# Kernel optimization log

Measured on AMD Instinct MI355X. Metric: run time of the kernel, lower is better.

Reference implementation:

```python
import jax, jax.numpy as jnp
import numpy as np

B, N, PL = 8, 961, 50          # batch, sequence_len=(64-4)//2+1 squared, patch_len=3*4^2+2
HID = 200                       # int(4.0 * patch_len)
D, H, HD = 768, 12, 64          # embed_dim, num_heads, head_dim
MP = 1536                       # int(2.0 * embed_dim)


def setup_inputs() -> dict:
    key = jax.random.key(0)
    ks = jax.random.split(key, 16)
    w = lambda k, i, o: jax.random.normal(k, (i, o), jnp.float32) / np.float32(np.sqrt(i))
    b = lambda k, o: jax.random.normal(k, (o,), jnp.float32) * np.float32(0.01)
    return {
        "x": jax.random.normal(ks[0], (B, N, PL), jnp.float32),
        "W1": w(ks[1], PL, HID),   "b1": b(ks[2], HID),
        "W2": w(ks[3], HID, HID),  "b2": b(ks[4], HID),
        "W3": w(ks[5], HID, HID),  "b3": b(ks[6], HID),
        "W4": w(ks[7], HID, D),    "b4": b(ks[8], D),
        "Wruv": w(ks[9], D, 3 * D), "bruv": b(ks[10], 3 * D),
        "Wp1": w(ks[11], N * HD, MP), "bp1": b(ks[12], MP),
        "Wp2": w(ks[13], MP, 1),      "bp2": b(ks[14], 1),
    }


def reference(x, W1, b1, W2, b2, W3, b3, W4, b4, Wruv, bruv, Wp1, bp1, Wp2, bp2):
    Bs, Ns, _ = x.shape
    # pointwise MLP (note: original has NO activations, just stacked Linears)
    h = x.reshape(Bs * Ns, -1)
    h = (((h @ W1 + b1) @ W2 + b2) @ W3 + b3) @ W4 + b4           # (B*N, D)
    # fused r,u,v projection -> (3, H, B, N, HD)
    ruv = (h @ Wruv + bruv).reshape(Bs, Ns, 3, H, HD).transpose(2, 3, 0, 1, 4)
    r, u, v = ruv[0], ruv[1], ruv[2]                               # each (H, B, N, HD)
    attn = jax.nn.softmax(jnp.einsum('hbnd,hbmd->hbnm', r, u), axis=-1)
    o = jnp.einsum('hbnm,hbmd->hbnd', attn, v).reshape(H, Bs, Ns * HD)
    # per-head projection: weights are SHARED across heads (list built via [m]*H)
    q = (jnp.einsum('hbm,mp->hbp', o, Wp1) + bp1) @ Wp2 + bp2      # (H, B, 1)
    return q[..., 0].T                                             # (B, 12)
```

## Files before the change

### kernel.cpp

```cpp
#include <hip/hip_runtime.h>
#include <hip/hip_bf16.h>

#define TPB 256

typedef __attribute__((ext_vector_type(8))) short bf16x8;
typedef __attribute__((ext_vector_type(4))) float f32x4;

static __device__ __forceinline__ unsigned short f2bf(float f) {
  union { float f; unsigned int u; } x; x.f = f;
  unsigned int r = x.u + 0x7FFF + ((x.u >> 16) & 1);
  return (unsigned short)(r >> 16);
}
static __device__ __forceinline__ float bf2f(unsigned short h) {
  union { unsigned int u; float f; } x; x.u = ((unsigned int)h) << 16;
  return x.f;
}

#define MFMA16(a, b, c) __builtin_amdgcn_mfma_f32_16x16x32_bf16(a, b, c, 0, 0, 0)

__global__ __launch_bounds__(TPB) void gemm_fold_k(
    const float* __restrict__ A, const float* __restrict__ lastrow,
    const float* __restrict__ W, const float* __restrict__ bias,
    float* __restrict__ C, int K, int Nc)
{
  __shared__ float As[16][68];
  __shared__ float Ws[16][68];
  int tid = threadIdx.x;
  int col0 = blockIdx.x * 64;
  int ty = tid >> 4, tx = tid & 15;
  float acc[4][4] = {};
  for (int k0 = 0; k0 < K; k0 += 16) {
#pragma unroll
    for (int i = 0; i < 4; ++i) {
      int idx = tid + i * 256;
      int r = idx >> 4, kk = idx & 15;
      int gk = k0 + kk;
      float v = 0.f;
      if (gk < K) {
        if (r < 50) v = A[(size_t)r * K + gk];
        else if (r == 50) v = lastrow[gk];
      }
      As[kk][r] = v;
    }
#pragma unroll
    for (int i = 0; i < 4; ++i) {
      int idx = tid + i * 256;
      int c = idx & 63, kk = idx >> 6;
      int gc = col0 + c, gk = k0 + kk;
      float v = 0.f;
      if (gk < K && gc < Nc) v = W[(size_t)gk * Nc + gc];
      Ws[kk][c] = v;
    }
    __syncthreads();
#pragma unroll
    for (int kk = 0; kk < 16; ++kk) {
      float4 a4 = *(const float4*)&As[kk][ty * 4];
      float4 b4 = *(const float4*)&Ws[kk][tx * 4];
      float av[4] = {a4.x, a4.y, a4.z, a4.w};
      float bv[4] = {b4.x, b4.y, b4.z, b4.w};
#pragma unroll
      for (int i = 0; i < 4; ++i)
#pragma unroll
        for (int j = 0; j < 4; ++j)
          acc[i][j] = fmaf(av[i], bv[j], acc[i][j]);
    }
    __syncthreads();
  }
#pragma unroll
  for (int i = 0; i < 4; ++i) {
    int gr = ty * 4 + i;
    if (gr >= 51) continue;
#pragma unroll
    for (int j = 0; j < 4; ++j) {
      int gc = col0 + tx * 4 + j;
      if (gc >= Nc) continue;
      float v = acc[i][j];
      if (gr == 50) v += bias[gc];
      C[(size_t)gr * Nc + gc] = v;
    }
  }
}

__global__ __launch_bounds__(TPB) void fold4_xprep_k(
    const float* __restrict__ aug3,
    const float* __restrict__ Wruv,
    const float* __restrict__ bruv,
    unsigned short* __restrict__ WfTh, unsigned short* __restrict__ WfTl,
    float* __restrict__ bfv,
    const float* __restrict__ x,
    unsigned short* __restrict__ xh, unsigned short* __restrict__ xl)
{
  __shared__ float As[16][68];
  __shared__ float Ws[16][68];
  int bid = blockIdx.x;
  int tid = threadIdx.x;

  if (bid >= 36) {
    int row0 = (bid - 36) * 64;
#pragma unroll
    for (int i = 0; i < 16; ++i) {
      int idx = tid + i * 256;
      int row = row0 + (idx >> 6), cc = idx & 63;
      if (row >= 7688) continue;
      float v = (cc < 50) ? x[(size_t)row * 50 + cc] : 0.f;
      unsigned short hi = f2bf(v);
      xh[(size_t)row * 64 + cc] = hi;
      xl[(size_t)row * 64 + cc] = f2bf(v - bf2f(hi));
    }
    return;
  }

  const int K = 768, Nc = 2304;
  const float* lastrow = aug3 + (size_t)50 * 768;
  int col0 = bid * 64;
  int ty = tid >> 4, tx = tid & 15;
  float acc[4][4] = {};
  for (int k0 = 0; k0 < K; k0 += 16) {
#pragma unroll
    for (int i = 0; i < 4; ++i) {
      int idx = tid + i * 256;
      int r = idx >> 4, kk = idx & 15;
      int gk = k0 + kk;
      float v = 0.f;
      if (r < 50) v = aug3[(size_t)r * K + gk];
      else if (r == 50) v = lastrow[gk];
      As[kk][r] = v;
    }
#pragma unroll
    for (int i = 0; i < 4; ++i) {
      int idx = tid + i * 256;
      int c = idx & 63, kk = idx >> 6;
      Ws[kk][c] = Wruv[(size_t)(k0 + kk) * Nc + col0 + c];
    }
    __syncthreads();
#pragma unroll
    for (int kk = 0; kk < 16; ++kk) {
      float4 a4 = *(const float4*)&As[kk][ty * 4];
      float4 b4 = *(const float4*)&Ws[kk][tx * 4];
      float av[4] = {a4.x, a4.y, a4.z, a4.w};
      float bv[4] = {b4.x, b4.y, b4.z, b4.w};
#pragma unroll
      for (int i = 0; i < 4; ++i)
#pragma unroll
        for (int j = 0; j < 4; ++j)
          acc[i][j] = fmaf(av[i], bv[j], acc[i][j]);
    }
    __syncthreads();
  }
#pragma unroll
  for (int i = 0; i < 4; ++i) {
    int gr = ty * 4 + i;
    if (gr >= 51) continue;
#pragma unroll
    for (int j = 0; j < 4; ++j) {
      int gc = col0 + tx * 4 + j;
      float v = acc[i][j];
      if (gr == 50) {
        bfv[gc] = v + bruv[gc];
      } else {
        unsigned short hi = f2bf(v);
        size_t el = (size_t)gc * 64 + gr;
        WfTh[el] = hi;
        WfTl[el] = f2bf(v - bf2f(hi));
      }
    }
  }
}

__global__ __launch_bounds__(TPB) void gemm_ruv_mfma_k(
    const unsigned short* __restrict__ xh,
    const unsigned short* __restrict__ xl,
    const unsigned short* __restrict__ WfTh,
    const unsigned short* __restrict__ WfTl,
    const float* __restrict__ bias,
    unsigned short* __restrict__ RU,
    unsigned short* __restrict__ Vt)
{
  int tid = threadIdx.x, w = tid >> 6, lane = tid & 63;
  int g = lane >> 4, c = lane & 15;
  int by = blockIdx.y;
  int b = by >> 4, nb = by & 15;
  int m0 = b * 961 + nb * 64;
  int n0base = nb * 64;
  int col0 = blockIdx.x * 256;
  int wc0 = w * 64;

  bf16x8 afh[4][2], afl[4][2];
#pragma unroll
  for (int rt = 0; rt < 4; ++rt) {
    size_t rowb = (size_t)(m0 + rt * 16 + c) * 64;
#pragma unroll
    for (int kk = 0; kk < 2; ++kk) {
      afh[rt][kk] = *(const bf16x8*)&xh[rowb + kk * 32 + g * 8];
      afl[rt][kk] = *(const bf16x8*)&xl[rowb + kk * 32 + g * 8];
    }
  }

  f32x4 zero4 = {0.f, 0.f, 0.f, 0.f};
  f32x4 acc[4][4] = {{zero4, zero4, zero4, zero4}, {zero4, zero4, zero4, zero4},
                     {zero4, zero4, zero4, zero4}, {zero4, zero4, zero4, zero4}};

#pragma unroll
  for (int ct = 0; ct < 4; ++ct) {
    size_t bcolb = (size_t)(col0 + wc0 + ct * 16 + c) * 64;
    bf16x8 bh0 = *(const bf16x8*)&WfTh[bcolb + g * 8];
    bf16x8 bh1 = *(const bf16x8*)&WfTh[bcolb + 32 + g * 8];
    bf16x8 bl0 = *(const bf16x8*)&WfTl[bcolb + g * 8];
    bf16x8 bl1 = *(const bf16x8*)&WfTl[bcolb + 32 + g * 8];
#pragma unroll
    for (int rt = 0; rt < 4; ++rt) {
      acc[rt][ct] = MFMA16(afh[rt][0], bh0, acc[rt][ct]);
      acc[rt][ct] = MFMA16(afh[rt][1], bh1, acc[rt][ct]);
      acc[rt][ct] = MFMA16(afl[rt][0], bh0, acc[rt][ct]);
      acc[rt][ct] = MFMA16(afl[rt][1], bh1, acc[rt][ct]);
      acc[rt][ct] = MFMA16(afh[rt][0], bl0, acc[rt][ct]);
      acc[rt][ct] = MFMA16(afh[rt][1], bl1, acc[rt][ct]);
    }
  }

  bool isRU = (col0 < 1536);
#pragma unroll
  for (int ct = 0; ct < 4; ++ct) {
    int col = col0 + wc0 + ct * 16 + c;
    float bs = bias[col];
    if (isRU) {
#pragma unroll
      for (int rt = 0; rt < 4; ++rt) {
        int lr0 = rt * 16 + g * 4;
#pragma unroll
        for (int r = 0; r < 4; ++r) {
          int n = n0base + lr0 + r;
          if (n <= 960)
            RU[(size_t)(m0 + lr0 + r) * 1536 + col] = f2bf(acc[rt][ct][r] + bs);
        }
      }
    } else {
      int hd = col - 1536;
      int hh = hd >> 6, d = hd & 63;
      size_t vrow = ((size_t)(hh * 8 + b) * 64 + d) * 968;
#pragma unroll
      for (int rt = 0; rt < 4; ++rt) {
        int n0 = n0base + rt * 16 + g * 4;
        if (n0 + 3 <= 960) {
          ushort4 o;
          o.x = f2bf(acc[rt][ct][0] + bs);
          o.y = f2bf(acc[rt][ct][1] + bs);
          o.z = f2bf(acc[rt][ct][2] + bs);
          o.w = f2bf(acc[rt][ct][3] + bs);
          *(ushort4*)&Vt[vrow + n0] = o;
        } else {
#pragma unroll
          for (int r = 0; r < 4; ++r) {
            int n = n0 + r;
            if (n <= 960) Vt[vrow + n] = f2bf(acc[rt][ct][r] + bs);
          }
        }
      }
    }
  }
}

__global__ __launch_bounds__(512) void fold_wp_init_k(
    const float* __restrict__ Wp1, const float* __restrict__ Wp2,
    float* __restrict__ wfold,
    const float* __restrict__ bp1, const float* __restrict__ bp2,
    float* __restrict__ out)
{
  __shared__ float w2[1536];
  __shared__ float red[8];
  int bid = blockIdx.x;
  int tid = threadIdx.x;
  int wv = tid >> 6, lane = tid & 63;

  if (bid == 7688) {
    float s = 0.f;
    for (int i = tid; i < 1536; i += 512) s += bp1[i] * Wp2[i];
#pragma unroll
    for (int off = 32; off >= 1; off >>= 1) s += __shfl_xor(s, off, 64);
    if (lane == 0) red[wv] = s;
    __syncthreads();
    if (tid < 96) {
      float tot = red[0] + red[1] + red[2] + red[3] +
                  red[4] + red[5] + red[6] + red[7] + bp2[0];
      out[tid] = tot;
    }
    return;
  }

  for (int i = tid; i < 1536; i += 512) w2[i] = Wp2[i];
  __syncthreads();
  int m = bid * 8 + wv;
  const float* row = Wp1 + (size_t)m * 1536;
  float s = 0.f;
#pragma unroll
  for (int k = 0; k < 6; ++k) {
    float4 a  = *(const float4*)(row + k * 256 + lane * 4);
    float4 ww = *(const float4*)&w2[k * 256 + lane * 4];
    s += a.x * ww.x + a.y * ww.y + a.z * ww.z + a.w * ww.w;
  }
#pragma unroll
  for (int off = 32; off >= 1; off >>= 1) s += __shfl_xor(s, off, 64);
  if (lane == 0) wfold[m] = s;
}

__global__ __launch_bounds__(512) void attn_final_k(
    const unsigned short* __restrict__ RU,
    const unsigned short* __restrict__ Vt,
    const float* __restrict__ wfold,
    float* __restrict__ out)
{
  __shared__ unsigned short sh[24576];
  int bid = blockIdx.x;
  int tid = threadIdx.x;

  const int NS = 961, RS = 1536, VROW = 968;
  int qb = bid & 7, hb = bid >> 3;
  int h = hb >> 3, b = hb & 7;
  int n0 = qb * 128;
  int w = tid >> 6, lane = tid & 63;
  int g = lane >> 4, c = lane & 15;
  const unsigned short* rubase = RU + (size_t)b * NS * RS;
  int roff = h * 64, uoff = 768 + h * 64;
  const unsigned short* vtbase = Vt + (size_t)hb * 64 * VROW;
  unsigned short* Kbuf[2] = {sh, sh + 4096};
  unsigned short* Vbuf[2] = {sh + 8192, sh + 12288};
  unsigned short* pw = sh + 16384 + w * 1024;

  int qrow = n0 + w * 16 + c;
  if (qrow > 960) qrow = 960;
  bf16x8 qf0 = *(const bf16x8*)(rubase + (size_t)qrow * RS + roff + g * 8);
  bf16x8 qf1 = *(const bf16x8*)(rubase + (size_t)qrow * RS + roff + 32 + g * 8);

  bf16x8 ones;
#pragma unroll
  for (int i = 0; i < 8; ++i) ones[i] = (short)0x3F80;

  int srow = tid >> 3, ss = tid & 7;
  int sel = srow * 64 + 8 * (ss ^ (srow & 7));
  const unsigned short* ksrc = rubase + uoff + ss * 8;
  const unsigned short* vsrc = vtbase + (size_t)srow * VROW + ss * 8;

  {
    int4 kv = *(const int4*)(ksrc + (size_t)srow * RS);
    int4 vv = *(const int4*)(vsrc);
    *(int4*)&Kbuf[0][sel] = kv;
    *(int4*)&Vbuf[0][sel] = vv;
  }
  __syncthreads();

  f32x4 zero4 = {0.f, 0.f, 0.f, 0.f};
  f32x4 oacc[4] = {zero4, zero4, zero4, zero4};
  f32x4 rowacc = zero4;

  unsigned short* Kc = Kbuf[0];
  unsigned short* Vc = Vbuf[0];
  unsigned short* Kn = Kbuf[1];
  unsigned short* Vn = Vbuf[1];

  for (int kt = 0; kt < 16; ++kt) {
    int4 pk, pv;
    bool pre = (kt < 15);
    if (pre) {
      int keyg = (kt + 1) * 64 + srow;
      int kcl = keyg > 960 ? 960 : keyg;
      pk = *(const int4*)(ksrc + (size_t)kcl * RS);
      pv = *(const int4*)(vsrc + (kt + 1) * 64);
    }

    f32x4 sa[4] = {zero4, zero4, zero4, zero4};
    __builtin_amdgcn_s_setprio(1);
#pragma unroll
    for (int ct = 0; ct < 4; ++ct) {
      int key = c * 4 + ct;
      int sw = (key & 7) * 8;
      bf16x8 k0 = *(const bf16x8*)&Kc[key * 64 + ((g * 8) ^ sw)];
      bf16x8 k1 = *(const bf16x8*)&Kc[key * 64 + ((32 + g * 8) ^ sw)];
      sa[ct] = MFMA16(qf0, k0, sa[ct]);
      sa[ct] = MFMA16(qf1, k1, sa[ct]);
    }
    __builtin_amdgcn_s_setprio(0);

    if (kt < 15) {
#pragma unroll
      for (int r = 0; r < 4; ++r) {
        unsigned short pb[4];
#pragma unroll
        for (int ct = 0; ct < 4; ++ct)
          pb[ct] = f2bf(__expf(sa[ct][r]));
        int q = g * 4 + r;
        int e0 = (c * 4) ^ ((q & 7) * 8);
        *(unsigned int*)&pw[q * 64 + e0] =
            (unsigned int)pb[0] | ((unsigned int)pb[1] << 16);
        *(unsigned int*)&pw[q * 64 + e0 + 2] =
            (unsigned int)pb[2] | ((unsigned int)pb[3] << 16);
      }
    } else {
#pragma unroll
      for (int r = 0; r < 4; ++r) {
        unsigned short pb[4];
#pragma unroll
        for (int ct = 0; ct < 4; ++ct) {
          int keyg = kt * 64 + c * 4 + ct;
          pb[ct] = (keyg <= 960) ? f2bf(__expf(sa[ct][r])) : (unsigned short)0;
        }
        int q = g * 4 + r;
        int e0 = (c * 4) ^ ((q & 7) * 8);
        *(unsigned int*)&pw[q * 64 + e0] =
            (unsigned int)pb[0] | ((unsigned int)pb[1] << 16);
        *(unsigned int*)&pw[q * 64 + e0 + 2] =
            (unsigned int)pb[2] | ((unsigned int)pb[3] << 16);
      }
    }

    if (pre) {
      *(int4*)&Kn[sel] = pk;
      *(int4*)&Vn[sel] = pv;
    }

    __builtin_amdgcn_s_setprio(1);
#pragma unroll
    for (int kk = 0; kk < 2; ++kk) {
      bf16x8 pa = *(const bf16x8*)&pw[c * 64 + ((kk * 32 + g * 8) ^ ((c & 7) * 8))];
      rowacc = MFMA16(pa, ones, rowacc);
#pragma unroll
      for (int dt = 0; dt < 4; ++dt) {
        int d = dt * 16 + c;
        bf16x8 vf = *(const bf16x8*)&Vc[d * 64 + ((kk * 32 + g * 8) ^ ((d & 7) * 8))];
        oacc[dt] = MFMA16(pa, vf, oacc[dt]);
      }
    }
    __builtin_amdgcn_s_setprio(0);

    __syncthreads();
    unsigned short* t;
    t = Kc; Kc = Kn; Kn = t;
    t = Vc; Vc = Vn; Vn = t;
  }

  int nbase = n0 + w * 16 + g * 4;
  float part = 0.f;
#pragma unroll
  for (int r = 0; r < 4; ++r) {
    int n = nbase + r;
    if (n > 960) continue;
    float inv = 1.f / rowacc[r];
#pragma unroll
    for (int dt = 0; dt < 4; ++dt)
      part += oacc[dt][r] * inv * wfold[(size_t)n * 64 + dt * 16 + c];
  }
#pragma unroll
  for (int off = 32; off >= 1; off >>= 1) part += __shfl_xor(part, off, 64);
  float* red = (float*)sh;
  if (lane == 0) red[w] = part;
  __syncthreads();
  if (tid == 0) {
    float tot = red[0] + red[1] + red[2] + red[3] +
                red[4] + red[5] + red[6] + red[7];
    atomicAdd(&out[b * 12 + h], tot);
  }
}

extern "C" void kernel_launch(void* const* d_in, const int* in_sizes, int n_in,
                              void* d_out, int out_size, void* d_ws, size_t ws_size,
                              hipStream_t stream)
{
  const float* x    = (const float*)d_in[0];
  const float* W1   = (const float*)d_in[1];
  const float* b1   = (const float*)d_in[2];
  const float* W2   = (const float*)d_in[3];
  const float* b2   = (const float*)d_in[4];
  const float* W3   = (const float*)d_in[5];
  const float* b3   = (const float*)d_in[6];
  const float* W4   = (const float*)d_in[7];
  const float* b4   = (const float*)d_in[8];
  const float* Wruv = (const float*)d_in[9];
  const float* bruv = (const float*)d_in[10];
  const float* Wp1  = (const float*)d_in[11];
  const float* bp1  = (const float*)d_in[12];
  const float* Wp2  = (const float*)d_in[13];
  const float* bp2  = (const float*)d_in[14];
  float* out = (float*)d_out;

  char* base = (char*)d_ws;
  size_t off = 0;
  auto alloc = [&](size_t bytes) -> void* {
    void* p = base + off;
    off = (off + bytes + 255) & ~(size_t)255;
    return p;
  };
  unsigned short* RU  = (unsigned short*)alloc((size_t)7688 * 1536 * 2);
  unsigned short* Vt  = (unsigned short*)alloc((size_t)96 * 64 * 968 * 2 + 1024);
  float* aug1  = (float*)alloc(51 * 200 * 4);
  float* aug2  = (float*)alloc(51 * 200 * 4);
  float* aug3  = (float*)alloc(51 * 768 * 4);
  unsigned short* WfTh = (unsigned short*)alloc((size_t)2304 * 64 * 2);
  unsigned short* WfTl = (unsigned short*)alloc((size_t)2304 * 64 * 2);
  unsigned short* xh   = (unsigned short*)alloc((size_t)(7688 + 64) * 64 * 2);
  unsigned short* xl   = (unsigned short*)alloc((size_t)(7688 + 64) * 64 * 2);
  float* bfv   = (float*)alloc(2304 * 4);
  float* wfold = (float*)alloc(61504 * 4);
  if (off > ws_size) return;

  dim3 tb(TPB);

  gemm_fold_k<<<dim3(4),  tb, 0, stream>>>(W1,   b1,            W2, b2, aug1, 200, 200);
  gemm_fold_k<<<dim3(4),  tb, 0, stream>>>(aug1, aug1 + 50*200, W3, b3, aug2, 200, 200);
  gemm_fold_k<<<dim3(12), tb, 0, stream>>>(aug2, aug2 + 50*200, W4, b4, aug3, 200, 768);

  fold4_xprep_k<<<dim3(157), tb, 0, stream>>>(aug3, Wruv, bruv, WfTh, WfTl, bfv, x, xh, xl);

  gemm_ruv_mfma_k<<<dim3(9, 128), tb, 0, stream>>>(xh, xl, WfTh, WfTl, bfv, RU, Vt);

  fold_wp_init_k<<<dim3(7689), dim3(512), 0, stream>>>(Wp1, Wp2, wfold, bp1, bp2, out);

  attn_final_k<<<dim3(768), dim3(512), 0, stream>>>(RU, Vt, wfold, out);
}
```

Baseline: 383.4 us.

## Spread Wp1·Wp2 fold across the small fold GEMM launches and enlarge K tiles

The standalone Wp1×Wp2 folding kernel is removed. Its rows are split into chunks and handled by extra blocks appended to the three weight-fold GEMM launches and the fold4/xprep launch, so the bandwidth-bound Wp1 read runs alongside the tiny latency-bound GEMMs that previously left most CUs idle. The fold GEMMs also move from a K-tile of 16 to 64, which means fewer barriers but more shared memory per block (about 35 KB). The bias/out init moves into the first launch; 4-wave blocks now handle 4 rows each, so the fold work needs more blocks.

```diff
diff --git a/kernel.cpp b/kernel.cpp
--- a/kernel.cpp
+++ b/kernel.cpp
@@ -18,22 +18,59 @@
 
 #define MFMA16(a, b, c) __builtin_amdgcn_mfma_f32_16x16x32_bf16(a, b, c, 0, 0, 0)
 
-__global__ __launch_bounds__(TPB) void gemm_fold_k(
+__global__ __launch_bounds__(TPB) void fold_wp_fused_k(
     const float* __restrict__ A, const float* __restrict__ lastrow,
     const float* __restrict__ W, const float* __restrict__ bias,
-    float* __restrict__ C, int K, int Nc)
+    float* __restrict__ C, int K, int Nc, int gemmBlocks,
+    const float* __restrict__ Wp1, const float* __restrict__ Wp2,
+    float* __restrict__ wfold, int wpStart, int wpCount,
+    const float* __restrict__ bp1, const float* __restrict__ bp2,
+    float* __restrict__ out)
 {
-  __shared__ float As[16][68];
-  __shared__ float Ws[16][68];
-  int tid = threadIdx.x;
-  int col0 = blockIdx.x * 64;
+  __shared__ float As[64][68];
+  __shared__ float Ws[64][68];
+  __shared__ float red[4];
+  int bid = blockIdx.x, tid = threadIdx.x;
+
+  if (bid >= gemmBlocks) {
+    int u = bid - gemmBlocks;
+    int wv = tid >> 6, lane = tid & 63;
+    if (u >= wpCount) {
+      float s = 0.f;
+      for (int i = tid; i < 1536; i += TPB) s += bp1[i] * Wp2[i];
+#pragma unroll
+      for (int off = 32; off >= 1; off >>= 1) s += __shfl_xor(s, off, 64);
+      if (lane == 0) red[wv] = s;
+      __syncthreads();
+      if (tid < 96) out[tid] = red[0] + red[1] + red[2] + red[3] + bp2[0];
+      return;
+    }
+    float* w2 = &As[0][0];
+    for (int i = tid; i < 1536; i += TPB) w2[i] = Wp2[i];
+    __syncthreads();
+    int m = (wpStart + u) * 4 + wv;
+    const float* row = Wp1 + (size_t)m * 1536;
+    float s = 0.f;
+#pragma unroll
+    for (int k = 0; k < 6; ++k) {
+      float4 a  = *(const float4*)(row + k * 256 + lane * 4);
+      float4 ww = *(const float4*)&w2[k * 256 + lane * 4];
+      s += a.x * ww.x + a.y * ww.y + a.z * ww.z + a.w * ww.w;
+    }
+#pragma unroll
+    for (int off = 32; off >= 1; off >>= 1) s += __shfl_xor(s, off, 64);
+    if (lane == 0) wfold[m] = s;
+    return;
+  }
+
+  int col0 = bid * 64;
   int ty = tid >> 4, tx = tid & 15;
   float acc[4][4] = {};
-  for (int k0 = 0; k0 < K; k0 += 16) {
-#pragma unroll
-    for (int i = 0; i < 4; ++i) {
-      int idx = tid + i * 256;
-      int r = idx >> 4, kk = idx & 15;
+  for (int k0 = 0; k0 < K; k0 += 64) {
+#pragma unroll
+    for (int i = 0; i < 16; ++i) {
+      int idx = tid + i * TPB;
+      int r = idx >> 6, kk = idx & 63;
       int gk = k0 + kk;
       float v = 0.f;
       if (gk < K) {
@@ -43,17 +80,17 @@
       As[kk][r] = v;
     }
 #pragma unroll
-    for (int i = 0; i < 4; ++i) {
-      int idx = tid + i * 256;
-      int c = idx & 63, kk = idx >> 6;
-      int gc = col0 + c, gk = k0 + kk;
+    for (int i = 0; i < 16; ++i) {
+      int idx = tid + i * TPB;
+      int kk = idx >> 6, cc = idx & 63;
+      int gk = k0 + kk, gc = col0 + cc;
       float v = 0.f;
       if (gk < K && gc < Nc) v = W[(size_t)gk * Nc + gc];
-      Ws[kk][c] = v;
-    }
-    __syncthreads();
-#pragma unroll
-    for (int kk = 0; kk < 16; ++kk) {
+      Ws[kk][cc] = v;
+    }
+    __syncthreads();
+#pragma unroll 8
+    for (int kk = 0; kk < 64; ++kk) {
       float4 a4 = *(const float4*)&As[kk][ty * 4];
       float4 b4 = *(const float4*)&Ws[kk][tx * 4];
       float av[4] = {a4.x, a4.y, a4.z, a4.w};
@@ -81,25 +118,48 @@
   }
 }
 
-__global__ __launch_bounds__(TPB) void fold4_xprep_k(
+__global__ __launch_bounds__(TPB) void fold4_fused_k(
     const float* __restrict__ aug3,
     const float* __restrict__ Wruv,
     const float* __restrict__ bruv,
     unsigned short* __restrict__ WfTh, unsigned short* __restrict__ WfTl,
     float* __restrict__ bfv,
     const float* __restrict__ x,
-    unsigned short* __restrict__ xh, unsigned short* __restrict__ xl)
+    unsigned short* __restrict__ xh, unsigned short* __restrict__ xl,
+    const float* __restrict__ Wp1, const float* __restrict__ Wp2,
+    float* __restrict__ wfold, int wpStart, int wpCount)
 {
-  __shared__ float As[16][68];
-  __shared__ float Ws[16][68];
-  int bid = blockIdx.x;
-  int tid = threadIdx.x;
+  __shared__ float As[64][68];
+  __shared__ float Ws[64][68];
+  int bid = blockIdx.x, tid = threadIdx.x;
+
+  if (bid >= 157) {
+    int u = bid - 157;
+    if (u >= wpCount) return;
+    int wv = tid >> 6, lane = tid & 63;
+    float* w2 = &As[0][0];
+    for (int i = tid; i < 1536; i += TPB) w2[i] = Wp2[i];
+    __syncthreads();
+    int m = (wpStart + u) * 4 + wv;
+    const float* row = Wp1 + (size_t)m * 1536;
+    float s = 0.f;
+#pragma unroll
+    for (int k = 0; k < 6; ++k) {
+      float4 a  = *(const float4*)(row + k * 256 + lane * 4);
+      float4 ww = *(const float4*)&w2[k * 256 + lane * 4];
+      s += a.x * ww.x + a.y * ww.y + a.z * ww.z + a.w * ww.w;
+    }
+#pragma unroll
+    for (int off = 32; off >= 1; off >>= 1) s += __shfl_xor(s, off, 64);
+    if (lane == 0) wfold[m] = s;
+    return;
+  }
 
   if (bid >= 36) {
     int row0 = (bid - 36) * 64;
 #pragma unroll
     for (int i = 0; i < 16; ++i) {
-      int idx = tid + i * 256;
+      int idx = tid + i * TPB;
       int row = row0 + (idx >> 6), cc = idx & 63;
       if (row >= 7688) continue;
       float v = (cc < 50) ? x[(size_t)row * 50 + cc] : 0.f;
@@ -115,11 +175,11 @@
   int col0 = bid * 64;
   int ty = tid >> 4, tx = tid & 15;
   float acc[4][4] = {};
-  for (int k0 = 0; k0 < K; k0 += 16) {
-#pragma unroll
-    for (int i = 0; i < 4; ++i) {
-      int idx = tid + i * 256;
-      int r = idx >> 4, kk = idx & 15;
+  for (int k0 = 0; k0 < K; k0 += 64) {
+#pragma unroll
+    for (int i = 0; i < 16; ++i) {
+      int idx = tid + i * TPB;
+      int r = idx >> 6, kk = idx & 63;
       int gk = k0 + kk;
       float v = 0.f;
       if (r < 50) v = aug3[(size_t)r * K + gk];
@@ -127,14 +187,14 @@
       As[kk][r] = v;
     }
 #pragma unroll
-    for (int i = 0; i < 4; ++i) {
-      int idx = tid + i * 256;
-      int c = idx & 63, kk = idx >> 6;
-      Ws[kk][c] = Wruv[(size_t)(k0 + kk) * Nc + col0 + c];
-    }
-    __syncthreads();
-#pragma unroll
-    for (int kk = 0; kk < 16; ++kk) {
+    for (int i = 0; i < 16; ++i) {
+      int idx = tid + i * TPB;
+      int kk = idx >> 6, cc = idx & 63;
+      Ws[kk][cc] = Wruv[(size_t)(k0 + kk) * Nc + col0 + cc];
+    }
+    __syncthreads();
+#pragma unroll 8
+    for (int kk = 0; kk < 64; ++kk) {
       float4 a4 = *(const float4*)&As[kk][ty * 4];
       float4 b4 = *(const float4*)&Ws[kk][tx * 4];
       float av[4] = {a4.x, a4.y, a4.z, a4.w};
@@ -258,49 +318,6 @@
       }
     }
   }
-}
-
-__global__ __launch_bounds__(512) void fold_wp_init_k(
-    const float* __restrict__ Wp1, const float* __restrict__ Wp2,
-    float* __restrict__ wfold,
-    const float* __restrict__ bp1, const float* __restrict__ bp2,
-    float* __restrict__ out)
-{
-  __shared__ float w2[1536];
-  __shared__ float red[8];
-  int bid = blockIdx.x;
-  int tid = threadIdx.x;
-  int wv = tid >> 6, lane = tid & 63;
-
-  if (bid == 7688) {
-    float s = 0.f;
-    for (int i = tid; i < 1536; i += 512) s += bp1[i] * Wp2[i];
-#pragma unroll
-    for (int off = 32; off >= 1; off >>= 1) s += __shfl_xor(s, off, 64);
-    if (lane == 0) red[wv] = s;
-    __syncthreads();
-    if (tid < 96) {
-      float tot = red[0] + red[1] + red[2] + red[3] +
-                  red[4] + red[5] + red[6] + red[7] + bp2[0];
-      out[tid] = tot;
-    }
-    return;
-  }
-
-  for (int i = tid; i < 1536; i += 512) w2[i] = Wp2[i];
-  __syncthreads();
-  int m = bid * 8 + wv;
-  const float* row = Wp1 + (size_t)m * 1536;
-  float s = 0.f;
-#pragma unroll
-  for (int k = 0; k < 6; ++k) {
-    float4 a  = *(const float4*)(row + k * 256 + lane * 4);
-    float4 ww = *(const float4*)&w2[k * 256 + lane * 4];
-    s += a.x * ww.x + a.y * ww.y + a.z * ww.z + a.w * ww.w;
-  }
-#pragma unroll
-  for (int off = 32; off >= 1; off >>= 1) s += __shfl_xor(s, off, 64);
-  if (lane == 0) wfold[m] = s;
 }
 
 __global__ __launch_bounds__(512) void attn_final_k(
@@ -503,15 +520,21 @@
 
   dim3 tb(TPB);
 
-  gemm_fold_k<<<dim3(4),  tb, 0, stream>>>(W1,   b1,            W2, b2, aug1, 200, 200);
-  gemm_fold_k<<<dim3(4),  tb, 0, stream>>>(aug1, aug1 + 50*200, W3, b3, aug2, 200, 200);
-  gemm_fold_k<<<dim3(12), tb, 0, stream>>>(aug2, aug2 + 50*200, W4, b4, aug3, 200, 768);
-
-  fold4_xprep_k<<<dim3(157), tb, 0, stream>>>(aug3, Wruv, bruv, WfTh, WfTl, bfv, x, xh, xl);
+  fold_wp_fused_k<<<dim3(4 + 3000 + 1), tb, 0, stream>>>(
+      W1, b1, W2, b2, aug1, 200, 200, 4,
+      Wp1, Wp2, wfold, 0, 3000, bp1, bp2, out);
+  fold_wp_fused_k<<<dim3(4 + 3000), tb, 0, stream>>>(
+      aug1, aug1 + 50 * 200, W3, b3, aug2, 200, 200, 4,
+      Wp1, Wp2, wfold, 3000, 3000, bp1, bp2, out);
+  fold_wp_fused_k<<<dim3(12 + 3000), tb, 0, stream>>>(
+      aug2, aug2 + 50 * 200, W4, b4, aug3, 200, 768, 12,
+      Wp1, Wp2, wfold, 6000, 3000, bp1, bp2, out);
+
+  fold4_fused_k<<<dim3(157 + 6376), tb, 0, stream>>>(
+      aug3, Wruv, bruv, WfTh, WfTl, bfv, x, xh, xl,
+      Wp1, Wp2, wfold, 9000, 6376);
 
   gemm_ruv_mfma_k<<<dim3(9, 128), tb, 0, stream>>>(xh, xl, WfTh, WfTl, bfv, RU, Vt);
 
-  fold_wp_init_k<<<dim3(7689), dim3(512), 0, stream>>>(Wp1, Wp2, wfold, bp1, bp2, out);
-
   attn_final_k<<<dim3(768), dim3(512), 0, stream>>>(RU, Vt, wfold, out);
 }
```

Result: faster. 329.8 us (-14.0%).
